# Kernel optimization log

Measured on AMD Instinct MI355X. Metric: run time of the kernel, lower is better.

## Reference

```python
import jax, jax.numpy as jnp
import numpy as np

N = 30000          # nodes
R = 8              # relations
NUM_BASES = 30     # basis decomposition (fixed in module)
IN_DIM = 256
Z_DIM = 128
HID = Z_DIM * 2
E = N * 16         # edges (avg degree 16)


def setup_inputs() -> dict:
    key = jax.random.key(0)
    ks = jax.random.split(key, 12)
    x = jax.random.normal(ks[0], (N, IN_DIM), jnp.float32)
    edge_index = jax.random.randint(ks[1], (2, E), 0, N, dtype=jnp.int64)
    edge_type = jax.random.randint(ks[2], (E,), 0, R, dtype=jnp.int64)
    s1 = 1.0 / np.sqrt(IN_DIM)
    s2 = 1.0 / np.sqrt(HID)
    sb = 1.0 / np.sqrt(NUM_BASES)
    bases1 = jax.random.normal(ks[3], (NUM_BASES, IN_DIM, HID), jnp.float32) * s1
    comp1 = jax.random.normal(ks[4], (R, NUM_BASES), jnp.float32) * sb
    root1 = jax.random.normal(ks[5], (IN_DIM, HID), jnp.float32) * s1
    bias1 = jnp.zeros((HID,), jnp.float32)
    bases2 = jax.random.normal(ks[6], (NUM_BASES, HID, Z_DIM), jnp.float32) * s2
    comp2 = jax.random.normal(ks[7], (R, NUM_BASES), jnp.float32) * sb
    root2 = jax.random.normal(ks[8], (HID, Z_DIM), jnp.float32) * s2
    bias2 = jnp.zeros((Z_DIM,), jnp.float32)
    return dict(x=x, edge_index=edge_index, edge_type=edge_type,
                bases1=bases1, comp1=comp1, root1=root1, bias1=bias1,
                bases2=bases2, comp2=comp2, root2=root2, bias2=bias2)


def _rgcn_layer(x, src, dst, etype, bases, comp, root, bias):
    # weight[r] = sum_b comp[r,b] * bases[b]  (basis decomposition)
    n = x.shape[0]
    W = jnp.einsum('rb,bio->rio', comp, bases)          # [R, in, out]
    xall = jnp.einsum('ni,rio->nro', x, W)              # [N, R, out] dense transform
    msg = xall[src, etype]                              # [E, out] gather per edge
    seg = dst * R + etype                               # segment = (dst, relation)
    sums = jax.ops.segment_sum(msg, seg, num_segments=n * R)
    cnt = jax.ops.segment_sum(jnp.ones((msg.shape[0],), msg.dtype), seg,
                              num_segments=n * R)
    mean = sums / jnp.maximum(cnt, 1.0)[:, None]        # PyG RGCNConv aggr='mean'
    agg = mean.reshape(n, R, -1).sum(axis=1)            # sum over relations
    return agg + x @ root + bias


def reference(x, edge_index, edge_type, bases1, comp1, root1, bias1,
              bases2, comp2, root2, bias2):
    src, dst = edge_index[0], edge_index[1]
    z = _rgcn_layer(x, src, dst, edge_type, bases1, comp1, root1, bias1)
    z = jax.nn.leaky_relu(z, negative_slope=0.01)
    z = _rgcn_layer(z, src, dst, edge_type, bases2, comp2, root2, bias2)
    return z
```

## Files before the change

### kernel.cpp

```cpp
#include <hip/hip_runtime.h>
#include <hip/hip_bf16.h>
#include <stdint.h>

#define NN     30000
#define MPAD   30080
#define RR     8
#define NBASES 30
#define KD     256
#define EE     480000
#define NSEG   (NN * RR)
#define K1     2048
#define KTOT   2304
#define BK     64
#define CAP    32

typedef unsigned short u16;
typedef __attribute__((ext_vector_type(8))) short bf16x8;
typedef __attribute__((ext_vector_type(4))) float f32x4;

__device__ __forceinline__ u16 f2b(float f) {
  union { float f; uint32_t u; } v; v.f = f;
  return (u16)((v.u + 0x7fffu + ((v.u >> 16) & 1u)) >> 16);
}
__device__ __forceinline__ float b2f(u16 h) {
  union { uint32_t u; float f; } v; v.u = ((uint32_t)h) << 16;
  return v.f;
}

__device__ __forceinline__ void gl_lds16(const void* g, void* l) {
  __builtin_amdgcn_global_load_lds((__attribute__((address_space(1))) void*)g,
                                   (__attribute__((address_space(3))) void*)l,
                                   16, 0, 0);
}

template<int NT, bool LAST>
__global__ __launch_bounds__(256)
void k_gemm4w(const u16* __restrict__ A1, const u16* __restrict__ A2,
              const u16* __restrict__ BT, const float* __restrict__ bias,
              u16* __restrict__ ob, float* __restrict__ of) {
  constexpr int NI = NT / 32;
  __shared__ u16 Alds[64 * BK];
  __shared__ u16 Blds[NT * BK];
  const int tid = threadIdx.x;
  const int w = tid >> 6, lane = tid & 63;
  const int bn = blockIdx.x * NT, bm = blockIdx.y * 64;
  const int wm = (w >> 1) * 32;
  const int wn = (w & 1) * (NT / 2);
  const int l15 = lane & 15, l4 = lane >> 4;

  f32x4 zero4 = {0.f, 0.f, 0.f, 0.f};
  f32x4 acc[2][NI];
  #pragma unroll
  for (int mi = 0; mi < 2; ++mi)
    #pragma unroll
    for (int ni = 0; ni < NI; ++ni) acc[mi][ni] = zero4;

  for (int k0 = 0; k0 < KTOT; k0 += BK) {
    #pragma unroll
    for (int it = 0; it < 2; ++it) {
      int chb = it * 256 + w * 64;
      int ch = chb + lane;
      int row = ch >> 3, pc = ch & 7;
      int lc = pc ^ (row & 7);
      const u16* src = (k0 < K1)
          ? &A1[(size_t)(bm + row) * K1 + k0 + lc * 8]
          : &A2[(size_t)(bm + row) * KD + (k0 - K1) + lc * 8];
      gl_lds16(src, &Alds[(size_t)chb * 8]);
    }
    #pragma unroll
    for (int it = 0; it < NT / 32; ++it) {
      int chb = it * 256 + w * 64;
      int ch = chb + lane;
      int row = ch >> 3, pc = ch & 7;
      int lc = pc ^ (row & 7);
      gl_lds16(&BT[(size_t)(bn + row) * KTOT + k0 + lc * 8], &Blds[(size_t)chb * 8]);
    }
    __syncthreads();
    #pragma unroll
    for (int s = 0; s < 2; ++s) {
      bf16x8 av[2], bv[NI];
      #pragma unroll
      for (int mi = 0; mi < 2; ++mi) {
        int row = wm + mi * 16 + l15;
        int pc = (4 * s + l4) ^ (row & 7);
        av[mi] = *(const bf16x8*)&Alds[row * BK + pc * 8];
      }
      #pragma unroll
      for (int ni = 0; ni < NI; ++ni) {
        int row = wn + ni * 16 + l15;
        int pc = (4 * s + l4) ^ (row & 7);
        bv[ni] = *(const bf16x8*)&Blds[row * BK + pc * 8];
      }
      #pragma unroll
      for (int mi = 0; mi < 2; ++mi)
        #pragma unroll
        for (int ni = 0; ni < NI; ++ni)
          acc[mi][ni] = __builtin_amdgcn_mfma_f32_16x16x32_bf16(av[mi], bv[ni], acc[mi][ni], 0, 0, 0);
    }
    __syncthreads();
  }

  #pragma unroll
  for (int mi = 0; mi < 2; ++mi) {
    #pragma unroll
    for (int ni = 0; ni < NI; ++ni) {
      int col = bn + wn + ni * 16 + l15;
      float bb = bias[col];
      #pragma unroll
      for (int v = 0; v < 4; ++v) {
        int row = bm + wm + mi * 16 + l4 * 4 + v;
        float val = acc[mi][ni][v] + bb;
        if (!LAST) {
          val = val > 0.f ? val : 0.01f * val;
          ob[(size_t)row * KD + col] = f2b(val);
        } else if (row < NN) {
          of[(size_t)row * 128 + col] = val;
        }
      }
    }
  }
}

__global__ __launch_bounds__(256)
void k_mean(const u16* __restrict__ X, const int* __restrict__ cnt,
            const int* __restrict__ esrc, u16* __restrict__ H) {
  const int d = blockIdx.x;
  const int tid = threadIdx.x;
  const int r = tid >> 5;
  const int ln = tid & 31;
  const int s = (d << 3) + r;
  int n = cnt[s]; n = n < CAP ? n : CAP;
  const int base = s * CAP;

  float a0 = 0.f, a1 = 0.f, a2 = 0.f, a3 = 0.f;
  float a4 = 0.f, a5 = 0.f, a6 = 0.f, a7 = 0.f;
  #pragma unroll 1
  for (int e = 0; e < n; e += 2) {
    int s0 = esrc[base + e];
    bool has1 = (e + 1 < n);
    int s1 = has1 ? esrc[base + e + 1] : s0;
    uint4 v0 = *(const uint4*)&X[(size_t)s0 * KD + ln * 8];
    uint4 v1 = *(const uint4*)&X[(size_t)s1 * KD + ln * 8];
    a0 += b2f((u16)v0.x); a1 += b2f((u16)(v0.x >> 16));
    a2 += b2f((u16)v0.y); a3 += b2f((u16)(v0.y >> 16));
    a4 += b2f((u16)v0.z); a5 += b2f((u16)(v0.z >> 16));
    a6 += b2f((u16)v0.w); a7 += b2f((u16)(v0.w >> 16));
    float m = has1 ? 1.f : 0.f;
    a0 = fmaf(m, b2f((u16)v1.x), a0); a1 = fmaf(m, b2f((u16)(v1.x >> 16)), a1);
    a2 = fmaf(m, b2f((u16)v1.y), a2); a3 = fmaf(m, b2f((u16)(v1.y >> 16)), a3);
    a4 = fmaf(m, b2f((u16)v1.z), a4); a5 = fmaf(m, b2f((u16)(v1.z >> 16)), a5);
    a6 = fmaf(m, b2f((u16)v1.w), a6); a7 = fmaf(m, b2f((u16)(v1.w >> 16)), a7);
  }
  float sc = (n > 0) ? 1.f / (float)n : 0.f;
  uint4 o;
  o.x = ((uint32_t)f2b(a1 * sc) << 16) | (uint32_t)f2b(a0 * sc);
  o.y = ((uint32_t)f2b(a3 * sc) << 16) | (uint32_t)f2b(a2 * sc);
  o.z = ((uint32_t)f2b(a5 * sc) << 16) | (uint32_t)f2b(a4 * sc);
  o.w = ((uint32_t)f2b(a7 * sc) << 16) | (uint32_t)f2b(a6 * sc);
  *(uint4*)&H[(size_t)d * K1 + (r << 8) + ln * 8] = o;
}

__global__ void k_cast_x(const float* __restrict__ x, u16* __restrict__ xb) {
  int t = blockIdx.x * 256 + threadIdx.x;
  if (t < NN * KD / 4) {
    float4 v = ((const float4*)x)[t];
    union { u16 h[4]; uint2 u; } p;
    p.h[0] = f2b(v.x); p.h[1] = f2b(v.y); p.h[2] = f2b(v.z); p.h[3] = f2b(v.w);
    ((uint2*)xb)[t] = p.u;
  }
}

__global__ void k_combine1(const float* __restrict__ bases, const float* __restrict__ comp,
                           const float* __restrict__ root, u16* __restrict__ BT) {
  int k = blockIdx.x, o = threadIdx.x;
  float v;
  if (k < K1) {
    int r = k >> 8, i = k & 255;
    float acc = 0.f;
    #pragma unroll
    for (int b = 0; b < NBASES; ++b)
      acc += comp[r * NBASES + b] * bases[(size_t)b * 65536 + i * 256 + o];
    v = acc;
  } else {
    v = root[(k - K1) * 256 + o];
  }
  BT[(size_t)o * KTOT + k] = f2b(v);
}

__global__ void k_combine2(const float* __restrict__ bases, const float* __restrict__ comp,
                           const float* __restrict__ root, u16* __restrict__ BT) {
  int k = blockIdx.x, o = threadIdx.x;
  float v;
  if (k < K1) {
    int r = k >> 8, i = k & 255;
    float acc = 0.f;
    #pragma unroll
    for (int b = 0; b < NBASES; ++b)
      acc += comp[r * NBASES + b] * bases[(size_t)b * 32768 + i * 128 + o];
    v = acc;
  } else {
    v = root[(k - K1) * 128 + o];
  }
  BT[(size_t)o * KTOT + k] = f2b(v);
}

__global__ void k_bucket_fs(const int* __restrict__ ei, const int* __restrict__ ety,
                            int* __restrict__ cnt, int* __restrict__ esrc) {
  int e = blockIdx.x * 256 + threadIdx.x;
  if (e < EE) {
    int seg = ei[EE + e] * RR + ety[e];
    int pos = atomicAdd(&cnt[seg], 1);
    if (pos < CAP) esrc[seg * CAP + pos] = ei[e];
  }
}

extern "C" void kernel_launch(void* const* d_in, const int* in_sizes, int n_in,
                              void* d_out, int out_size, void* d_ws, size_t ws_size,
                              hipStream_t stream) {
  const float* x      = (const float*)d_in[0];
  const int*   ei     = (const int*)d_in[1];
  const int*   ety    = (const int*)d_in[2];
  const float* bases1 = (const float*)d_in[3];
  const float* comp1  = (const float*)d_in[4];
  const float* root1  = (const float*)d_in[5];
  const float* bias1  = (const float*)d_in[6];
  const float* bases2 = (const float*)d_in[7];
  const float* comp2  = (const float*)d_in[8];
  const float* root2  = (const float*)d_in[9];
  const float* bias2  = (const float*)d_in[10];
  float* out = (float*)d_out;

  char* p = (char*)d_ws;
  auto alloc = [&](size_t bytes) {
    char* q = p; p += (bytes + 255) & ~(size_t)255; return q;
  };
  u16* H    = (u16*)alloc((size_t)MPAD * K1 * 2);
  u16* xb   = (u16*)alloc((size_t)MPAD * KD * 2);
  u16* z1b  = (u16*)alloc((size_t)MPAD * KD * 2);
  u16* BT1  = (u16*)alloc((size_t)256 * KTOT * 2);
  u16* BT2  = (u16*)alloc((size_t)128 * KTOT * 2);
  int* cnt  = (int*)alloc((size_t)NSEG * 4);
  int* esrc = (int*)alloc((size_t)NSEG * CAP * 4);

  hipMemsetAsync(cnt, 0, (size_t)NSEG * 4, stream);
  k_bucket_fs<<<(EE + 255) / 256, 256, 0, stream>>>(ei, ety, cnt, esrc);

  k_cast_x<<<NN * KD / 4 / 256, 256, 0, stream>>>(x, xb);
  k_combine1<<<KTOT, 256, 0, stream>>>(bases1, comp1, root1, BT1);
  k_combine2<<<KTOT, 128, 0, stream>>>(bases2, comp2, root2, BT2);

  k_mean<<<NN, 256, 0, stream>>>(xb, cnt, esrc, H);
  k_gemm4w<256, false><<<dim3(1, 470), 256, 0, stream>>>(H, xb, BT1, bias1, z1b, nullptr);

  k_mean<<<NN, 256, 0, stream>>>(z1b, cnt, esrc, H);
  k_gemm4w<128, true><<<dim3(1, 470), 256, 0, stream>>>(H, z1b, BT2, bias2, nullptr, out);
}
```

Before: 361.4 us.

## Double-buffer GEMM LDS tiles with 8-wave blocks and narrower N tiles

Rewrites the fused GEMM to use 512-thread blocks (8 waves, each owning a 16-row slab) with LDS double buffering, so the global-to-LDS load of the next K tile is issued before computing the current one. The N tile is halved and the grid doubled along N, giving more blocks to spread across CUs. The aim is to hide global load latency and raise occupancy. In exchange, each wave does less MFMA work per LDS fragment read, and the A tile is fetched twice from global memory.

```diff
diff --git a/kernel.cpp b/kernel.cpp
--- a/kernel.cpp
+++ b/kernel.cpp
@@ -34,88 +34,86 @@
 }
 
 template<int NT, bool LAST>
-__global__ __launch_bounds__(256)
-void k_gemm4w(const u16* __restrict__ A1, const u16* __restrict__ A2,
+__global__ __launch_bounds__(512, 6)
+void k_gemm8w(const u16* __restrict__ A1, const u16* __restrict__ A2,
               const u16* __restrict__ BT, const float* __restrict__ bias,
               u16* __restrict__ ob, float* __restrict__ of) {
   constexpr int NI = NT / 32;
-  __shared__ u16 Alds[64 * BK];
-  __shared__ u16 Blds[NT * BK];
+  constexpr int NKI = KTOT / BK;
+  __shared__ u16 Alds[2][64 * BK];
+  __shared__ u16 Blds[2][NT * BK];
   const int tid = threadIdx.x;
   const int w = tid >> 6, lane = tid & 63;
   const int bn = blockIdx.x * NT, bm = blockIdx.y * 64;
-  const int wm = (w >> 1) * 32;
+  const int wm = (w >> 1) * 16;
   const int wn = (w & 1) * (NT / 2);
   const int l15 = lane & 15, l4 = lane >> 4;
 
-  f32x4 zero4 = {0.f, 0.f, 0.f, 0.f};
-  f32x4 acc[2][NI];
+  f32x4 acc[NI];
   #pragma unroll
-  for (int mi = 0; mi < 2; ++mi)
-    #pragma unroll
-    for (int ni = 0; ni < NI; ++ni) acc[mi][ni] = zero4;
-
-  for (int k0 = 0; k0 < KTOT; k0 += BK) {
-    #pragma unroll
-    for (int it = 0; it < 2; ++it) {
-      int chb = it * 256 + w * 64;
+  for (int ni = 0; ni < NI; ++ni) acc[ni] = (f32x4){0.f, 0.f, 0.f, 0.f};
+
+  auto stage = [&](int buf, int k0) {
+    {
+      int chb = w * 64;
       int ch = chb + lane;
       int row = ch >> 3, pc = ch & 7;
       int lc = pc ^ (row & 7);
       const u16* src = (k0 < K1)
           ? &A1[(size_t)(bm + row) * K1 + k0 + lc * 8]
           : &A2[(size_t)(bm + row) * KD + (k0 - K1) + lc * 8];
-      gl_lds16(src, &Alds[(size_t)chb * 8]);
-    }
-    #pragma unroll
-    for (int it = 0; it < NT / 32; ++it) {
-      int chb = it * 256 + w * 64;
+      gl_lds16(src, &Alds[buf][chb * 8]);
+    }
+    #pragma unroll
+    for (int it = 0; it < NT / 64; ++it) {
+      int chb = it * 512 + w * 64;
       int ch = chb + lane;
       int row = ch >> 3, pc = ch & 7;
       int lc = pc ^ (row & 7);
-      gl_lds16(&BT[(size_t)(bn + row) * KTOT + k0 + lc * 8], &Blds[(size_t)chb * 8]);
-    }
-    __syncthreads();
+      gl_lds16(&BT[(size_t)(bn + row) * KTOT + k0 + lc * 8], &Blds[buf][chb * 8]);
+    }
+  };
+
+  stage(0, 0);
+  __syncthreads();
+  int cur = 0;
+  for (int t = 0; t < NKI; ++t) {
+    if (t + 1 < NKI) stage(cur ^ 1, (t + 1) * BK);
     #pragma unroll
     for (int s = 0; s < 2; ++s) {
-      bf16x8 av[2], bv[NI];
-      #pragma unroll
-      for (int mi = 0; mi < 2; ++mi) {
-        int row = wm + mi * 16 + l15;
+      bf16x8 av, bv[NI];
+      {
+        int row = wm + l15;
         int pc = (4 * s + l4) ^ (row & 7);
-        av[mi] = *(const bf16x8*)&Alds[row * BK + pc * 8];
+        av = *(const bf16x8*)&Alds[cur][row * BK + pc * 8];
       }
       #pragma unroll
       for (int ni = 0; ni < NI; ++ni) {
         int row = wn + ni * 16 + l15;
         int pc = (4 * s + l4) ^ (row & 7);
-        bv[ni] = *(const bf16x8*)&Blds[row * BK + pc * 8];
+        bv[ni] = *(const bf16x8*)&Blds[cur][row * BK + pc * 8];
       }
       #pragma unroll
-      for (int mi = 0; mi < 2; ++mi)
-        #pragma unroll
-        for (int ni = 0; ni < NI; ++ni)
-          acc[mi][ni] = __builtin_amdgcn_mfma_f32_16x16x32_bf16(av[mi], bv[ni], acc[mi][ni], 0, 0, 0);
+      for (int ni = 0; ni < NI; ++ni)
+        acc[ni] = __builtin_amdgcn_mfma_f32_16x16x32_bf16(av, bv[ni], acc[ni], 0, 0, 0);
     }
     __syncthreads();
+    cur ^= 1;
   }
 
   #pragma unroll
-  for (int mi = 0; mi < 2; ++mi) {
-    #pragma unroll
-    for (int ni = 0; ni < NI; ++ni) {
-      int col = bn + wn + ni * 16 + l15;
-      float bb = bias[col];
-      #pragma unroll
-      for (int v = 0; v < 4; ++v) {
-        int row = bm + wm + mi * 16 + l4 * 4 + v;
-        float val = acc[mi][ni][v] + bb;
-        if (!LAST) {
-          val = val > 0.f ? val : 0.01f * val;
-          ob[(size_t)row * KD + col] = f2b(val);
-        } else if (row < NN) {
-          of[(size_t)row * 128 + col] = val;
-        }
+  for (int ni = 0; ni < NI; ++ni) {
+    int col = bn + wn + ni * 16 + l15;
+    float bb = bias[col];
+    #pragma unroll
+    for (int v = 0; v < 4; ++v) {
+      int row = bm + wm + l4 * 4 + v;
+      float val = acc[ni][v] + bb;
+      if (!LAST) {
+        val = val > 0.f ? val : 0.01f * val;
+        ob[(size_t)row * KD + col] = f2b(val);
+      } else if (row < NN) {
+        of[(size_t)row * 128 + col] = val;
       }
     }
   }
@@ -250,8 +248,8 @@
   k_combine2<<<KTOT, 128, 0, stream>>>(bases2, comp2, root2, BT2);
 
   k_mean<<<NN, 256, 0, stream>>>(xb, cnt, esrc, H);
-  k_gemm4w<256, false><<<dim3(1, 470), 256, 0, stream>>>(H, xb, BT1, bias1, z1b, nullptr);
+  k_gemm8w<128, false><<<dim3(2, 470), 512, 0, stream>>>(H, xb, BT1, bias1, z1b, nullptr);
 
   k_mean<<<NN, 256, 0, stream>>>(z1b, cnt, esrc, H);
-  k_gemm4w<128, true><<<dim3(1, 470), 256, 0, stream>>>(H, z1b, BT2, bias2, nullptr, out);
-}
+  k_gemm8w<64, true><<<dim3(2, 470), 512, 0, stream>>>(H, z1b, BT2, bias2, nullptr, out);
+}
```

After: 376.1 us. 1.04x slower.
